# Optimization experiments

Measured on AMD Instinct MI355X. Metric: run time of the kernel, lower is better.

The kernel has to match this reference:

```python
import jax, jax.numpy as jnp
import numpy as np

B, L, D, K = 16, 4096, 256, 64
RHO, LAMBDA_Q, LAMBDA_S = 0.5, 1.0, 1.0


def setup_inputs() -> dict:
    key = jax.random.key(0)
    ks = jax.random.split(key, 16)
    s = 1.0 / np.sqrt(D)
    inp = {
        'q': jax.random.normal(ks[0], (B, D), jnp.float32),
        'r_pos': jax.random.normal(ks[1], (B, D), jnp.float32),
        'r_neg': jax.random.normal(ks[2], (B, D), jnp.float32),
        'h': jax.random.normal(ks[3], (B, L, D), jnp.float32),
        'rp': jax.random.normal(ks[4], (B, L, D), jnp.float32),
        'rn': jax.random.normal(ks[5], (B, L, D), jnp.float32),
        'lengths': jnp.maximum(1, jax.random.randint(ks[6], (B,), 0, L, jnp.int32)),
        'proto_idx': 3,
        'prototypes': jax.random.normal(ks[7], (K, D), jnp.float32),
        'W_hist_w': jax.random.normal(ks[8], (D, 2 * D), jnp.float32) * s,
        'W_hist_b': jnp.zeros((D,), jnp.float32),
        'Wq_w': jax.random.normal(ks[9], (D, D), jnp.float32) * s,
        'Wq_b': jnp.zeros((D,), jnp.float32),
        'Ws_w': jax.random.normal(ks[10], (D, D), jnp.float32) * s,
        'Ws_b': jnp.zeros((D,), jnp.float32),
    }
    return inp


def reference(q, r_pos, r_neg, h, rp, rn, lengths, proto_idx, prototypes,
              W_hist_w, W_hist_b, Wq_w, Wq_b, Ws_w, Ws_b):
    d = q.shape[-1]
    scale = 1.0 / jnp.sqrt(jnp.asarray(d, q.dtype))
    a = prototypes[proto_idx]                                   # [d]
    # gather + tanh-MLP over padded events: inp = [h, rp-rn] -> [B,L,2d]
    inp = jnp.concatenate([h, rp - rn], axis=-1)
    o = jnp.tanh(jnp.einsum('ble,de->bld', inp, W_hist_w) + W_hist_b)  # [B,L,d]
    # attention logits against prototype and query
    logits = (jnp.einsum('bld,d->bl', o, a)
              + RHO * jnp.einsum('bld,bd->bl', o, q)) * scale   # [B,L]
    mask = jnp.arange(o.shape[1])[None, :] < lengths[:, None]   # [B,L]
    logits = jnp.where(mask, logits, -1e30)
    alpha = jax.nn.softmax(logits, axis=1)
    s_q = jnp.einsum('bl,bld->bd', alpha, o)                    # [B,d]
    z = (a[None, :]
         + LAMBDA_Q * (q @ Wq_w.T + Wq_b)
         + LAMBDA_S * (s_q @ Ws_w.T + Ws_b))                    # [B,d]
    delta = jnp.sum(z * (r_pos - r_neg), axis=-1)               # [B]
    # BCE-with-logits against all-ones targets: mean softplus(-delta)
    l_pair = jnp.mean(jax.nn.softplus(-delta))
    return l_pair
```

## Files before the change

kernel.cpp:

```cpp
#include <hip/hip_runtime.h>

#define B_      16
#define L_      4096
#define D_      256
#define K2_     512
#define TILE_M  64
#define BK      64
#define KITERS  8
#define PSTRIDE 264

typedef float f32x4 __attribute__((ext_vector_type(4)));
typedef short bf16x8 __attribute__((ext_vector_type(8)));

__device__ __forceinline__ unsigned short f2bf(float x) {
    unsigned int u = __float_as_uint(x);
    u += 0x7FFF + ((u >> 16) & 1);
    return (unsigned short)(u >> 16);
}

__device__ __forceinline__ void gload_lds16(const void* g, void* l) {
    __builtin_amdgcn_global_load_lds(
        (const __attribute__((address_space(1))) unsigned int*)g,
        (__attribute__((address_space(3))) unsigned int*)l, 16, 0, 0);
}

__global__ __launch_bounds__(256) void prep_kernel(
    const float* __restrict__ Wh, const float* __restrict__ protos,
    const float* __restrict__ q, const int* __restrict__ pidx,
    unsigned short* __restrict__ wsW, float* __restrict__ aeff)
{
    const int blk = blockIdx.x, tid = threadIdx.x;
    if (blk < 256) {
        int p  = blk * 256 + tid;
        int d  = p >> 8;
        int pe = p & 255;
        int e  = pe * 2;
        int t  = e >> 6;
        int kk = e & 63;
        float2 w = *reinterpret_cast<const float2*>(Wh + d * K2_ + e);
        unsigned int v = (unsigned int)f2bf(w.x) | ((unsigned int)f2bf(w.y) << 16);
        int dst = t * 32768 + ((d * 128 + kk * 2) ^ ((d & 7) << 4));
        *reinterpret_cast<unsigned int*>(reinterpret_cast<char*>(wsW) + dst) = v;
    } else {
        int b = blk - 256;
        int d = tid;
        int pi = pidx[0];
        aeff[b * D_ + d] = (protos[pi * D_ + d] + 0.5f * q[b * D_ + d]) * 0.0625f;
    }
}

__global__ __launch_bounds__(256, 2) void main_kernel(
    const float* __restrict__ h, const float* __restrict__ rp, const float* __restrict__ rn,
    const int* __restrict__ lengths, const unsigned short* __restrict__ wsW,
    const float* __restrict__ aeff, const float* __restrict__ bhist,
    float* __restrict__ partials)
{
    const int bid = blockIdx.x;
    const int b   = bid >> 6;
    const int t   = bid & 63;
    const int len = lengths[b];
    const int l0  = t * TILE_M;
    if (l0 >= len) return;

    __shared__ __align__(16) unsigned short Albs[TILE_M * BK];
    __shared__ __align__(16) unsigned short Blbs[D_ * BK];
    __shared__ float red[4 * TILE_M];
    __shared__ float pbuf[TILE_M];

    const int tid  = threadIdx.x;
    const int lane = tid & 63;
    const int wv   = tid >> 6;
    const int r16  = lane & 15;
    const int kg   = lane >> 4;

    const int ar  = tid >> 2;
    const int akk = (tid & 3) * 16;

    const f32x4 zero4 = {0.f, 0.f, 0.f, 0.f};
    f32x4 acc[4][4];
#pragma unroll
    for (int m = 0; m < 4; ++m)
#pragma unroll
        for (int n = 0; n < 4; ++n) acc[m][n] = zero4;

    char* Ab = reinterpret_cast<char*>(Albs);
    char* Bb = reinterpret_cast<char*>(Blbs);

    for (int tk = 0; tk < KITERS; ++tk) {
        const char* bsrc = reinterpret_cast<const char*>(wsW) + tk * 32768;
#pragma unroll
        for (int i = 0; i < 8; ++i) {
            int off = i * 4096 + wv * 1024;
            gload_lds16(bsrc + off + lane * 16, Bb + off);
        }
        {
            float vals[16];
            if (tk < 4) {
                const float* src = h + ((size_t)(b * L_ + l0 + ar)) * D_ + tk * 64 + akk;
#pragma unroll
                for (int i = 0; i < 4; ++i) {
                    float4 v = reinterpret_cast<const float4*>(src)[i];
                    vals[i*4+0] = v.x; vals[i*4+1] = v.y; vals[i*4+2] = v.z; vals[i*4+3] = v.w;
                }
            } else {
                size_t o0 = ((size_t)(b * L_ + l0 + ar)) * D_ + (tk - 4) * 64 + akk;
                const float* sp = rp + o0;
                const float* sn = rn + o0;
#pragma unroll
                for (int i = 0; i < 4; ++i) {
                    float4 vp = reinterpret_cast<const float4*>(sp)[i];
                    float4 vn = reinterpret_cast<const float4*>(sn)[i];
                    vals[i*4+0] = vp.x - vn.x; vals[i*4+1] = vp.y - vn.y;
                    vals[i*4+2] = vp.z - vn.z; vals[i*4+3] = vp.w - vn.w;
                }
            }
            unsigned int pk[8];
#pragma unroll
            for (int i = 0; i < 8; ++i)
                pk[i] = (unsigned int)f2bf(vals[2*i]) | ((unsigned int)f2bf(vals[2*i+1]) << 16);
            int s0 = (ar * 128 + akk * 2) ^ ((ar & 7) << 4);
            int s1 = (ar * 128 + akk * 2 + 16) ^ ((ar & 7) << 4);
            *reinterpret_cast<uint4*>(Ab + s0) = make_uint4(pk[0], pk[1], pk[2], pk[3]);
            *reinterpret_cast<uint4*>(Ab + s1) = make_uint4(pk[4], pk[5], pk[6], pk[7]);
        }
        __syncthreads();

#pragma unroll
        for (int ks = 0; ks < 2; ++ks) {
            const int kk = ks * 32 + kg * 8;
            bf16x8 af[4], bf[4];
#pragma unroll
            for (int m = 0; m < 4; ++m) {
                int row = m * 16 + r16;
                int off = (row * 128 + kk * 2) ^ ((row & 7) << 4);
                af[m] = *reinterpret_cast<const bf16x8*>(Ab + off);
            }
#pragma unroll
            for (int n = 0; n < 4; ++n) {
                int d = wv * 64 + n * 16 + r16;
                int off = (d * 128 + kk * 2) ^ ((d & 7) << 4);
                bf[n] = *reinterpret_cast<const bf16x8*>(Bb + off);
            }
#pragma unroll
            for (int m = 0; m < 4; ++m)
#pragma unroll
                for (int n = 0; n < 4; ++n)
                    acc[m][n] = __builtin_amdgcn_mfma_f32_16x16x32_bf16(af[m], bf[n], acc[m][n], 0, 0, 0);
        }
        __syncthreads();
    }

    float av[4], bh[4];
#pragma unroll
    for (int n = 0; n < 4; ++n) {
        int col = wv * 64 + n * 16 + r16;
        av[n] = aeff[b * D_ + col];
        bh[n] = bhist[col];
    }
    float part[4][4];
#pragma unroll
    for (int m = 0; m < 4; ++m)
#pragma unroll
        for (int rg = 0; rg < 4; ++rg) part[m][rg] = 0.f;
#pragma unroll
    for (int m = 0; m < 4; ++m)
#pragma unroll
        for (int n = 0; n < 4; ++n)
#pragma unroll
            for (int rg = 0; rg < 4; ++rg) {
                float o = tanhf(acc[m][n][rg] + bh[n]);
                acc[m][n][rg] = o;
                part[m][rg] += o * av[n];
            }
#pragma unroll
    for (int off = 1; off < 16; off <<= 1)
#pragma unroll
        for (int m = 0; m < 4; ++m)
#pragma unroll
            for (int rg = 0; rg < 4; ++rg)
                part[m][rg] += __shfl_xor(part[m][rg], off, 64);
    if (r16 == 0) {
#pragma unroll
        for (int m = 0; m < 4; ++m)
#pragma unroll
            for (int rg = 0; rg < 4; ++rg)
                red[wv * 64 + m * 16 + kg * 4 + rg] = part[m][rg];
    }
    __syncthreads();

    float* pout = partials + (size_t)(b * 64 + t) * PSTRIDE;
    if (tid < 64) {
        int row = tid;
        float lg = red[row] + red[64 + row] + red[128 + row] + red[192 + row];
        bool valid = (l0 + row) < len;
        float mv = valid ? lg : -3.0e38f;
#pragma unroll
        for (int off = 1; off < 64; off <<= 1)
            mv = fmaxf(mv, __shfl_xor(mv, off, 64));
        float p = valid ? __expf(lg - mv) : 0.f;
        float sa = p;
#pragma unroll
        for (int off = 1; off < 64; off <<= 1)
            sa += __shfl_xor(sa, off, 64);
        pbuf[row] = p;
        if (tid == 0) { pout[0] = mv; pout[1] = sa; }
    }
    __syncthreads();

    float so[4] = {0.f, 0.f, 0.f, 0.f};
#pragma unroll
    for (int m = 0; m < 4; ++m)
#pragma unroll
        for (int rg = 0; rg < 4; ++rg) {
            float p = pbuf[m * 16 + kg * 4 + rg];
#pragma unroll
            for (int n = 0; n < 4; ++n)
                so[n] += p * acc[m][n][rg];
        }
#pragma unroll
    for (int n = 0; n < 4; ++n) {
        so[n] += __shfl_xor(so[n], 16, 64);
        so[n] += __shfl_xor(so[n], 32, 64);
    }
    if (lane < 16) {
#pragma unroll
        for (int n = 0; n < 4; ++n)
            pout[2 + wv * 64 + n * 16 + lane] = so[n];
    }
}

__global__ __launch_bounds__(256) void reduce_kernel(
    const float* __restrict__ partials, const int* __restrict__ lengths,
    const float* __restrict__ protos, const int* __restrict__ pidx,
    const float* __restrict__ q,
    const float* __restrict__ Wq_w, const float* __restrict__ Wq_b,
    const float* __restrict__ Ws_w, const float* __restrict__ Ws_b,
    const float* __restrict__ rpos, const float* __restrict__ rneg,
    float* __restrict__ out)
{
    const int b   = blockIdx.x;
    const int tid = threadIdx.x;
    const int len = lengths[b];
    const int nT  = (len + TILE_M - 1) / TILE_M;

    __shared__ __align__(16) float mArr[64];
    __shared__ __align__(16) float sAArr[64];
    __shared__ __align__(16) float sq[D_];
    __shared__ __align__(16) float qlds[D_];
    __shared__ float wsum[4];

    const float* pbase = partials + (size_t)b * 64 * PSTRIDE;
    if (tid < nT) {
        mArr[tid]  = pbase[(size_t)tid * PSTRIDE];
        sAArr[tid] = pbase[(size_t)tid * PSTRIDE + 1];
    }
    qlds[tid] = q[b * D_ + tid];
    __syncthreads();

    float M = -3.0e38f;
    for (int t = 0; t < nT; ++t) M = fmaxf(M, mArr[t]);
    float den = 0.f, num = 0.f;
    for (int t = 0; t < nT; ++t) {
        float f = __expf(mArr[t] - M);
        den += f * sAArr[t];
        num += f * pbase[(size_t)t * PSTRIDE + 2 + tid];
    }
    sq[tid] = num / den;
    __syncthreads();

    const int pi = pidx[0];
    float zd = protos[pi * D_ + tid] + Wq_b[tid] + Ws_b[tid];
    const float4* wqr = reinterpret_cast<const float4*>(Wq_w + (size_t)tid * D_);
    const float4* wsr = reinterpret_cast<const float4*>(Ws_w + (size_t)tid * D_);
    const float4* q4  = reinterpret_cast<const float4*>(qlds);
    const float4* s4  = reinterpret_cast<const float4*>(sq);
    float accq = 0.f, accs = 0.f;
#pragma unroll 4
    for (int e = 0; e < D_ / 4; ++e) {
        float4 wq = wqr[e], ws = wsr[e], qv = q4[e], sv = s4[e];
        accq += wq.x * qv.x + wq.y * qv.y + wq.z * qv.z + wq.w * qv.w;
        accs += ws.x * sv.x + ws.y * sv.y + ws.z * sv.z + ws.w * sv.w;
    }
    zd += accq + accs;

    float v = zd * (rpos[b * D_ + tid] - rneg[b * D_ + tid]);
#pragma unroll
    for (int off = 1; off < 64; off <<= 1) v += __shfl_xor(v, off, 64);
    if ((tid & 63) == 0) wsum[tid >> 6] = v;
    __syncthreads();
    if (tid == 0) {
        float delta = wsum[0] + wsum[1] + wsum[2] + wsum[3];
        float x = -delta;
        float sp = fmaxf(x, 0.f) + log1pf(__expf(-fabsf(x)));
        atomicAdd(out, sp * (1.0f / (float)B_));
    }
}

extern "C" void kernel_launch(void* const* d_in, const int* in_sizes, int n_in,
                              void* d_out, int out_size, void* d_ws, size_t ws_size,
                              hipStream_t stream) {
    const float* q       = (const float*)d_in[0];
    const float* r_pos   = (const float*)d_in[1];
    const float* r_neg   = (const float*)d_in[2];
    const float* h       = (const float*)d_in[3];
    const float* rp      = (const float*)d_in[4];
    const float* rn      = (const float*)d_in[5];
    const int*   lengths = (const int*)d_in[6];
    const int*   pidx    = (const int*)d_in[7];
    const float* protos  = (const float*)d_in[8];
    const float* Wh_w    = (const float*)d_in[9];
    const float* Wh_b    = (const float*)d_in[10];
    const float* Wq_w    = (const float*)d_in[11];
    const float* Wq_b    = (const float*)d_in[12];
    const float* Ws_w    = (const float*)d_in[13];
    const float* Ws_b    = (const float*)d_in[14];
    float* out = (float*)d_out;

    char* ws = (char*)d_ws;
    unsigned short* wsW = (unsigned short*)ws;
    float* aeff     = (float*)(ws + 262144);
    float* partials = (float*)(ws + 278528);

    hipMemsetAsync(out, 0, sizeof(float), stream);
    prep_kernel<<<dim3(272), dim3(256), 0, stream>>>(Wh_w, protos, q, pidx, wsW, aeff);
    main_kernel<<<dim3(B_ * 64), dim3(256), 0, stream>>>(h, rp, rn, lengths, wsW, aeff, Wh_b, partials);
    reduce_kernel<<<dim3(B_), dim3(256), 0, stream>>>(partials, lengths, protos, pidx, q,
                                                      Wq_w, Wq_b, Ws_w, Ws_b, r_pos, r_neg, out);
}
```

Measured before the change: 257.8 us.

## Double-buffer GEMM staging, use fast tanh, and coalesce reduce matvec

Main kernel now double-buffers the A and B tiles in one 80KB shared array. Loads for the next K step are issued before the MFMAs of the current step, so global and LDS staging overlap with compute. tanhf is replaced by an exp-based fast_tanh, and the reduce kernel's Wq/Ws matvec is rewritten so four lanes share a row and read it coalesced, then combine with shuffles. The larger shared footprint may cut occupancy below the requested two blocks per CU, and fast_tanh loses some accuracy.

Result: no change. 253.3 us (-1.7%).

```diff
diff --git a/kernel.cpp b/kernel.cpp
--- a/kernel.cpp
+++ b/kernel.cpp
@@ -24,6 +24,11 @@
         (__attribute__((address_space(3))) unsigned int*)l, 16, 0, 0);
 }
 
+__device__ __forceinline__ float fast_tanh(float x) {
+    float e = __expf(2.0f * x);
+    return 1.0f - __fdividef(2.0f, e + 1.0f);
+}
+
 __global__ __launch_bounds__(256) void prep_kernel(
     const float* __restrict__ Wh, const float* __restrict__ protos,
     const float* __restrict__ q, const int* __restrict__ pidx,
@@ -31,10 +36,8 @@
 {
     const int blk = blockIdx.x, tid = threadIdx.x;
     if (blk < 256) {
-        int p  = blk * 256 + tid;
-        int d  = p >> 8;
-        int pe = p & 255;
-        int e  = pe * 2;
+        int d  = blk;
+        int e  = tid * 2;
         int t  = e >> 6;
         int kk = e & 63;
         float2 w = *reinterpret_cast<const float2*>(Wh + d * K2_ + e);
@@ -62,10 +65,7 @@
     const int l0  = t * TILE_M;
     if (l0 >= len) return;
 
-    __shared__ __align__(16) unsigned short Albs[TILE_M * BK];
-    __shared__ __align__(16) unsigned short Blbs[D_ * BK];
-    __shared__ float red[4 * TILE_M];
-    __shared__ float pbuf[TILE_M];
+    __shared__ __align__(16) char SM[81920];
 
     const int tid  = threadIdx.x;
     const int lane = tid & 63;
@@ -75,6 +75,8 @@
 
     const int ar  = tid >> 2;
     const int akk = (tid & 3) * 16;
+    const int s0  = (ar * 128 + akk * 2) ^ ((ar & 7) << 4);
+    const int s1  = (ar * 128 + akk * 2 + 16) ^ ((ar & 7) << 4);
 
     const f32x4 zero4 = {0.f, 0.f, 0.f, 0.f};
     f32x4 acc[4][4];
@@ -83,48 +85,54 @@
 #pragma unroll
         for (int n = 0; n < 4; ++n) acc[m][n] = zero4;
 
-    char* Ab = reinterpret_cast<char*>(Albs);
-    char* Bb = reinterpret_cast<char*>(Blbs);
-
-    for (int tk = 0; tk < KITERS; ++tk) {
+    f32x4 ra[4], rb[4];
+
+    auto stageB = [&](int buf, int tk) {
         const char* bsrc = reinterpret_cast<const char*>(wsW) + tk * 32768;
+        char* dst = SM + 16384 + buf * 32768;
 #pragma unroll
         for (int i = 0; i < 8; ++i) {
             int off = i * 4096 + wv * 1024;
-            gload_lds16(bsrc + off + lane * 16, Bb + off);
-        }
-        {
-            float vals[16];
-            if (tk < 4) {
-                const float* src = h + ((size_t)(b * L_ + l0 + ar)) * D_ + tk * 64 + akk;
-#pragma unroll
-                for (int i = 0; i < 4; ++i) {
-                    float4 v = reinterpret_cast<const float4*>(src)[i];
-                    vals[i*4+0] = v.x; vals[i*4+1] = v.y; vals[i*4+2] = v.z; vals[i*4+3] = v.w;
-                }
-            } else {
-                size_t o0 = ((size_t)(b * L_ + l0 + ar)) * D_ + (tk - 4) * 64 + akk;
-                const float* sp = rp + o0;
-                const float* sn = rn + o0;
-#pragma unroll
-                for (int i = 0; i < 4; ++i) {
-                    float4 vp = reinterpret_cast<const float4*>(sp)[i];
-                    float4 vn = reinterpret_cast<const float4*>(sn)[i];
-                    vals[i*4+0] = vp.x - vn.x; vals[i*4+1] = vp.y - vn.y;
-                    vals[i*4+2] = vp.z - vn.z; vals[i*4+3] = vp.w - vn.w;
-                }
-            }
-            unsigned int pk[8];
-#pragma unroll
-            for (int i = 0; i < 8; ++i)
-                pk[i] = (unsigned int)f2bf(vals[2*i]) | ((unsigned int)f2bf(vals[2*i+1]) << 16);
-            int s0 = (ar * 128 + akk * 2) ^ ((ar & 7) << 4);
-            int s1 = (ar * 128 + akk * 2 + 16) ^ ((ar & 7) << 4);
-            *reinterpret_cast<uint4*>(Ab + s0) = make_uint4(pk[0], pk[1], pk[2], pk[3]);
-            *reinterpret_cast<uint4*>(Ab + s1) = make_uint4(pk[4], pk[5], pk[6], pk[7]);
-        }
-        __syncthreads();
-
+            gload_lds16(bsrc + off + lane * 16, dst + off);
+        }
+    };
+    auto loadA = [&](int tk) {
+        if (tk < 4) {
+            const float* src = h + ((size_t)(b * L_ + l0 + ar)) * D_ + tk * 64 + akk;
+#pragma unroll
+            for (int i = 0; i < 4; ++i) ra[i] = reinterpret_cast<const f32x4*>(src)[i];
+        } else {
+            size_t o0 = ((size_t)(b * L_ + l0 + ar)) * D_ + (tk - 4) * 64 + akk;
+#pragma unroll
+            for (int i = 0; i < 4; ++i) ra[i] = reinterpret_cast<const f32x4*>(rp + o0)[i];
+#pragma unroll
+            for (int i = 0; i < 4; ++i) rb[i] = reinterpret_cast<const f32x4*>(rn + o0)[i];
+        }
+    };
+    auto writeA = [&](int buf, int tk) {
+        float vals[16];
+        if (tk < 4) {
+#pragma unroll
+            for (int i = 0; i < 4; ++i)
+#pragma unroll
+                for (int j = 0; j < 4; ++j) vals[i * 4 + j] = ra[i][j];
+        } else {
+#pragma unroll
+            for (int i = 0; i < 4; ++i)
+#pragma unroll
+                for (int j = 0; j < 4; ++j) vals[i * 4 + j] = ra[i][j] - rb[i][j];
+        }
+        unsigned int pk[8];
+#pragma unroll
+        for (int i = 0; i < 8; ++i)
+            pk[i] = (unsigned int)f2bf(vals[2 * i]) | ((unsigned int)f2bf(vals[2 * i + 1]) << 16);
+        char* Ab = SM + buf * 8192;
+        *reinterpret_cast<uint4*>(Ab + s0) = make_uint4(pk[0], pk[1], pk[2], pk[3]);
+        *reinterpret_cast<uint4*>(Ab + s1) = make_uint4(pk[4], pk[5], pk[6], pk[7]);
+    };
+    auto computeT = [&](int buf) {
+        const char* Ab = SM + buf * 8192;
+        const char* Bb = SM + 16384 + buf * 32768;
 #pragma unroll
         for (int ks = 0; ks < 2; ++ks) {
             const int kk = ks * 32 + kg * 8;
@@ -147,8 +155,25 @@
                 for (int n = 0; n < 4; ++n)
                     acc[m][n] = __builtin_amdgcn_mfma_f32_16x16x32_bf16(af[m], bf[n], acc[m][n], 0, 0, 0);
         }
+    };
+
+    loadA(0);
+    stageB(0, 0);
+    writeA(0, 0);
+    __syncthreads();
+
+    int buf = 0;
+    for (int tk = 0; tk < KITERS; ++tk) {
+        const bool pf = (tk + 1) < KITERS;
+        if (pf) { stageB(buf ^ 1, tk + 1); loadA(tk + 1); }
+        computeT(buf);
+        if (pf) writeA(buf ^ 1, tk + 1);
         __syncthreads();
-    }
+        buf ^= 1;
+    }
+
+    float* red  = reinterpret_cast<float*>(SM);
+    float* pbuf = reinterpret_cast<float*>(SM + 1024);
 
     float av[4], bh[4];
 #pragma unroll
@@ -168,7 +193,7 @@
         for (int n = 0; n < 4; ++n)
 #pragma unroll
             for (int rg = 0; rg < 4; ++rg) {
-                float o = tanhf(acc[m][n][rg] + bh[n]);
+                float o = fast_tanh(acc[m][n][rg] + bh[n]);
                 acc[m][n][rg] = o;
                 part[m][rg] += o * av[n];
             }
@@ -240,6 +265,8 @@
 {
     const int b   = blockIdx.x;
     const int tid = threadIdx.x;
+    const int lane = tid & 63;
+    const int wv   = tid >> 6;
     const int len = lengths[b];
     const int nT  = (len + TILE_M - 1) / TILE_M;
 
@@ -247,6 +274,7 @@
     __shared__ __align__(16) float sAArr[64];
     __shared__ __align__(16) float sq[D_];
     __shared__ __align__(16) float qlds[D_];
+    __shared__ __align__(16) float zbuf[D_];
     __shared__ float wsum[4];
 
     const float* pbase = partials + (size_t)b * 64 * PSTRIDE;
@@ -268,25 +296,33 @@
     sq[tid] = num / den;
     __syncthreads();
 
+    const int c = lane & 3;
+    const float4* q4 = reinterpret_cast<const float4*>(qlds) + c * 16;
+    const float4* s4 = reinterpret_cast<const float4*>(sq) + c * 16;
+#pragma unroll
+    for (int p = 0; p < 4; ++p) {
+        int drow = p * 64 + wv * 16 + (lane >> 2);
+        const float4* wq4 = reinterpret_cast<const float4*>(Wq_w + (size_t)drow * D_) + c * 16;
+        const float4* ws4 = reinterpret_cast<const float4*>(Ws_w + (size_t)drow * D_) + c * 16;
+        float a = 0.f;
+#pragma unroll 4
+        for (int i = 0; i < 16; ++i) {
+            float4 wq = wq4[i], ws = ws4[i], qv = q4[i], sv = s4[i];
+            a += wq.x * qv.x + wq.y * qv.y + wq.z * qv.z + wq.w * qv.w;
+            a += ws.x * sv.x + ws.y * sv.y + ws.z * sv.z + ws.w * sv.w;
+        }
+        a += __shfl_xor(a, 1, 64);
+        a += __shfl_xor(a, 2, 64);
+        if (c == 0) zbuf[drow] = a;
+    }
+    __syncthreads();
+
     const int pi = pidx[0];
-    float zd = protos[pi * D_ + tid] + Wq_b[tid] + Ws_b[tid];
-    const float4* wqr = reinterpret_cast<const float4*>(Wq_w + (size_t)tid * D_);
-    const float4* wsr = reinterpret_cast<const float4*>(Ws_w + (size_t)tid * D_);
-    const float4* q4  = reinterpret_cast<const float4*>(qlds);
-    const float4* s4  = reinterpret_cast<const float4*>(sq);
-    float accq = 0.f, accs = 0.f;
-#pragma unroll 4
-    for (int e = 0; e < D_ / 4; ++e) {
-        float4 wq = wqr[e], ws = wsr[e], qv = q4[e], sv = s4[e];
-        accq += wq.x * qv.x + wq.y * qv.y + wq.z * qv.z + wq.w * qv.w;
-        accs += ws.x * sv.x + ws.y * sv.y + ws.z * sv.z + ws.w * sv.w;
-    }
-    zd += accq + accs;
-
+    float zd = protos[pi * D_ + tid] + Wq_b[tid] + Ws_b[tid] + zbuf[tid];
     float v = zd * (rpos[b * D_ + tid] - rneg[b * D_ + tid]);
 #pragma unroll
     for (int off = 1; off < 64; off <<= 1) v += __shfl_xor(v, off, 64);
-    if ((tid & 63) == 0) wsum[tid >> 6] = v;
+    if (lane == 0) wsum[wv] = v;
     __syncthreads();
     if (tid == 0) {
         float delta = wsum[0] + wsum[1] + wsum[2] + wsum[3];
```
